# Performance work log

Hardware: AMD Instinct MI355X
Metric: run time of the kernel (lower is better)

Reference implementation:

```python
import jax, jax.numpy as jnp
import numpy as np

NH = 8          # num_heads (init kwarg)
NUM_GROUPS = 32
EPS = 1e-5


def setup_inputs() -> dict:
    key = jax.random.key(0)
    ks = jax.random.split(key, 4)
    B, C, H, W = 2, 512, 64, 64
    x = jax.random.normal(ks[0], (B, C, H, W), dtype=jnp.float32)
    qkv_w = jax.random.normal(ks[1], (3 * C, C), dtype=jnp.float32) * (1.0 / np.sqrt(C))
    proj_w = jax.random.normal(ks[2], (C, C), dtype=jnp.float32) * (1.0 / np.sqrt(C))
    proj_b = jax.random.normal(ks[3], (C,), dtype=jnp.float32) * 0.02
    gn_w = jnp.ones((C,), dtype=jnp.float32)
    gn_b = jnp.zeros((C,), dtype=jnp.float32)
    return {"x": x, "qkv_w": qkv_w, "proj_w": proj_w, "proj_b": proj_b,
            "gn_w": gn_w, "gn_b": gn_b}


def _group_norm(x, gamma, beta):
    B, C, H, W = x.shape
    xg = x.reshape(B, NUM_GROUPS, C // NUM_GROUPS, H, W)
    mean = xg.mean(axis=(2, 3, 4), keepdims=True)
    var = xg.var(axis=(2, 3, 4), keepdims=True)
    xg = (xg - mean) * jax.lax.rsqrt(var + EPS)
    x = xg.reshape(B, C, H, W)
    return x * gamma[None, :, None, None] + beta[None, :, None, None]


def reference(x, qkv_w, proj_w, proj_b, gn_w, gn_b):
    B, C, H, W = x.shape
    h = _group_norm(x, gn_w, gn_b)
    # 1x1 conv == channel matmul
    qkv = jnp.einsum('oc,bchw->bohw', qkv_w, h)  # [B, 3C, H, W]
    # faithful legacy reshape: per-head contiguous [q,k,v] blocks of 3*C//NH channels
    qkv = qkv.reshape(B * NH, 3 * C // NH, H * W)
    q, k, v = jnp.split(qkv, 3, axis=1)          # each [B*NH, C//NH, HW]
    scale = 1.0 / np.sqrt(np.sqrt(C // NH))
    attn = jnp.einsum('bci,bcj->bij', q * scale, k * scale)  # [B*NH, HW, HW]
    attn = jax.nn.softmax(attn, axis=-1)
    hout = jnp.einsum('bij,bcj->bci', attn, v)   # [B*NH, C//NH, HW]
    hout = hout.reshape(B, C, H, W)
    hout = jnp.einsum('oc,bchw->bohw', proj_w, hout) + proj_b[None, :, None, None]
    return x + hout
```

## Files before the change

kernel.cpp:

```cpp
#include <hip/hip_runtime.h>
#include <math.h>

typedef __attribute__((ext_vector_type(8))) short short8;
typedef __attribute__((ext_vector_type(4))) float floatx4;
typedef __attribute__((ext_vector_type(16))) float floatx16;

__device__ __forceinline__ unsigned short f2bf(float f) {
  union { float f; unsigned int u; } v; v.f = f;
  unsigned int r = v.u + 0x7fffu + ((v.u >> 16) & 1u);
  return (unsigned short)(r >> 16);
}

__device__ __forceinline__ float bf2f(unsigned short h) {
  union { unsigned int u; float f; } v; v.u = ((unsigned int)h) << 16;
  return v.f;
}

__device__ __forceinline__ unsigned int pack2(unsigned short a, unsigned short b) {
  return (unsigned int)a | ((unsigned int)b << 16);
}

__device__ __forceinline__ float fast_exp2(float x) {
#if __has_builtin(__builtin_amdgcn_exp2f)
  return __builtin_amdgcn_exp2f(x);
#else
  return exp2f(x);
#endif
}

__device__ __forceinline__ void async16(const unsigned short* gp, unsigned short* lp) {
  __builtin_amdgcn_global_load_lds(
      (__attribute__((address_space(1))) void*)(gp),
      (__attribute__((address_space(3))) void*)(lp), 16, 0, 0);
}

__global__ void setup_kernel(const float* __restrict__ x, float2* __restrict__ stats_p,
                             const float* __restrict__ qkv_w, unsigned short* __restrict__ wqkv,
                             const float* __restrict__ proj_w, unsigned short* __restrict__ wproj) {
  if (blockIdx.x < 512) {
    const int bid = blockIdx.x;
    const int bg  = bid >> 3;
    const int sub = bid & 7;
    const float4* p = (const float4*)(x + (size_t)bg * 65536 + (size_t)sub * 8192);
    float s = 0.f, ss = 0.f;
    #pragma unroll
    for (int i = 0; i < 8; i++) {
      float4 v = p[threadIdx.x + i*256];
      s  += v.x + v.y + v.z + v.w;
      ss += v.x*v.x + v.y*v.y + v.z*v.z + v.w*v.w;
    }
    #pragma unroll
    for (int off = 32; off >= 1; off >>= 1) {
      s  += __shfl_xor(s,  off, 64);
      ss += __shfl_xor(ss, off, 64);
    }
    __shared__ float red[2][4];
    int wv = threadIdx.x >> 6;
    if ((threadIdx.x & 63) == 0) { red[0][wv] = s; red[1][wv] = ss; }
    __syncthreads();
    if (threadIdx.x == 0) {
      s  = red[0][0] + red[0][1] + red[0][2] + red[0][3];
      ss = red[1][0] + red[1][1] + red[1][2] + red[1][3];
      stats_p[bid] = make_float2(s, ss);
    }
  } else {
    int i = (blockIdx.x - 512) * 256 + threadIdx.x;
    const float* s; unsigned short* d;
    if (i < 196608) { s = qkv_w; d = wqkv; }
    else { i -= 196608; s = proj_w; d = wproj; }
    float4 vv = ((const float4*)s)[i];
    uint2 o;
    o.x = pack2(f2bf(vv.x), f2bf(vv.y));
    o.y = pack2(f2bf(vv.z), f2bf(vv.w));
    ((uint2*)d)[i] = o;
  }
}

__global__ void gn_apply_t(const float* __restrict__ x, const float2* __restrict__ stats_p,
                           const float* __restrict__ gw, const float* __restrict__ gb,
                           unsigned short* __restrict__ h_t) {
  __shared__ __align__(16) unsigned short tile[64][72];
  const int b = blockIdx.z, c0 = blockIdx.y * 64, hw0 = blockIdx.x * 64;
  const int t = threadIdx.x;
  {
    const int cl = t >> 2;
    const int hs = (t & 3) * 16;
    const int c  = c0 + cl;
    const int g  = c >> 4;
    const float2* sp = stats_p + ((size_t)(b*32 + g) << 3);
    float s = 0.f, ss = 0.f;
    #pragma unroll
    for (int k = 0; k < 8; k++) { float2 v = sp[k]; s += v.x; ss += v.y; }
    const float mean = s * (1.f/65536.f);
    const float var  = ss * (1.f/65536.f) - mean*mean;
    const float rstd = rsqrtf(var + 1e-5f);
    const float w  = gw[c] * rstd;
    const float bb = gb[c] - mean * w;
    const float4* src = (const float4*)(x + ((size_t)(b*512 + c))*4096 + hw0 + hs);
    #pragma unroll
    for (int i = 0; i < 4; i++) {
      float4 vv = src[i];
      unsigned short* d = &tile[cl][hs + i*4];
      d[0] = f2bf(vv.x*w + bb); d[1] = f2bf(vv.y*w + bb);
      d[2] = f2bf(vv.z*w + bb); d[3] = f2bf(vv.w*w + bb);
    }
  }
  __syncthreads();
  {
    const int hwl = t >> 2;
    const int cs  = (t & 3) * 16;
    uint4 w0, w1;
    w0.x = pack2(tile[cs+ 0][hwl], tile[cs+ 1][hwl]);
    w0.y = pack2(tile[cs+ 2][hwl], tile[cs+ 3][hwl]);
    w0.z = pack2(tile[cs+ 4][hwl], tile[cs+ 5][hwl]);
    w0.w = pack2(tile[cs+ 6][hwl], tile[cs+ 7][hwl]);
    w1.x = pack2(tile[cs+ 8][hwl], tile[cs+ 9][hwl]);
    w1.y = pack2(tile[cs+10][hwl], tile[cs+11][hwl]);
    w1.z = pack2(tile[cs+12][hwl], tile[cs+13][hwl]);
    w1.w = pack2(tile[cs+14][hwl], tile[cs+15][hwl]);
    unsigned short* dst = h_t + ((size_t)(b*4096 + hw0 + hwl))*512 + c0 + cs;
    *(uint4*)dst       = w0;
    *(uint4*)(dst + 8) = w1;
  }
}

__global__ __launch_bounds__(256, 3)
void qkv_gemm(const unsigned short* __restrict__ A,
              const unsigned short* __restrict__ Bt,
              unsigned short* __restrict__ q_t,
              unsigned short* __restrict__ k_t,
              unsigned short* __restrict__ v_) {
  __shared__ __align__(16) unsigned short As[128*32];
  __shared__ __align__(16) unsigned short Bs[128*32];
  const int b   = blockIdx.z;
  const int n0  = blockIdx.x * 128;
  const int o0  = blockIdx.y * 128;
  const int tid = threadIdx.x;
  const int wave = tid >> 6, lane = tid & 63;
  const int wr = wave >> 1, wc = wave & 1;
  const int fm = lane & 15, fq = lane >> 4;
  const int srow = lane >> 2, scol = (lane & 3) * 8;

  const unsigned short* Ab = A + (size_t)o0 * 512;
  const unsigned short* Bb = Bt + ((size_t)b*4096 + n0) * 512;

  bool vsw[4];
  #pragma unroll
  for (int fr = 0; fr < 4; fr++) {
    const int ob = o0 + wr*64 + fr*16;
    vsw[fr] = ((ob % 192) >> 6) == 2;
  }

  floatx4 acc[4][4];
  #pragma unroll
  for (int i = 0; i < 4; i++)
    #pragma unroll
    for (int j = 0; j < 4; j++) acc[i][j] = (floatx4){0.f,0.f,0.f,0.f};

  for (int k0 = 0; k0 < 512; k0 += 32) {
    __syncthreads();
    #pragma unroll
    for (int cc = 0; cc < 2; cc++) {
      int ch = wave*2 + cc;
      async16(Ab + (size_t)(ch*16 + srow)*512 + k0 + scol, &As[ch*512]);
      async16(Bb + (size_t)(ch*16 + srow)*512 + k0 + scol, &Bs[ch*512]);
    }
    __syncthreads();
    short8 af[4], bf[4];
    #pragma unroll
    for (int f = 0; f < 4; f++) {
      af[f] = *(const short8*)&As[(wr*64 + f*16 + fm)*32 + fq*8];
      bf[f] = *(const short8*)&Bs[(wc*64 + f*16 + fm)*32 + fq*8];
    }
    #pragma unroll
    for (int fr = 0; fr < 4; fr++) {
      if (vsw[fr]) {
        #pragma unroll
        for (int fc = 0; fc < 4; fc++)
          acc[fr][fc] = __builtin_amdgcn_mfma_f32_16x16x32_bf16(bf[fc], af[fr], acc[fr][fc], 0, 0, 0);
      } else {
        #pragma unroll
        for (int fc = 0; fc < 4; fc++)
          acc[fr][fc] = __builtin_amdgcn_mfma_f32_16x16x32_bf16(af[fr], bf[fc], acc[fr][fc], 0, 0, 0);
      }
    }
  }

  #pragma unroll
  for (int fr = 0; fr < 4; fr++) {
    const int ob     = o0 + wr*64 + fr*16;
    const int head   = ob / 192;
    const int rem    = ob % 192;
    const int region = rem >> 6;
    const int bhh    = b*8 + head;
    #pragma unroll
    for (int fc = 0; fc < 4; fc++) {
      if (region == 0) {
        const int i = n0 + wc*64 + fc*16 + fm;
        const int dsub = (rem & 63) + fq*4;
        unsigned short t4[4];
        #pragma unroll
        for (int r = 0; r < 4; r++) t4[r] = f2bf(acc[fr][fc][r] * 0.18033688f);
        uint2 o; o.x = pack2(t4[0], t4[1]); o.y = pack2(t4[2], t4[3]);
        *(uint2*)&q_t[((size_t)bhh*4096 + i)*64 + dsub] = o;
      } else if (region == 1) {
        const int i = n0 + wc*64 + fc*16 + fm;
        const int dsub = (rem & 63) + fq*4;
        unsigned short t4[4];
        #pragma unroll
        for (int r = 0; r < 4; r++) t4[r] = f2bf(acc[fr][fc][r]);
        uint2 o; o.x = pack2(t4[0], t4[1]); o.y = pack2(t4[2], t4[3]);
        *(uint2*)&k_t[((size_t)bhh*4096 + i)*64 + dsub] = o;
      } else {
        const int dsub = (rem & 63) + fm;
        const int tok0 = n0 + wc*64 + fc*16 + fq*4;
        unsigned short t4[4];
        #pragma unroll
        for (int r = 0; r < 4; r++) t4[r] = f2bf(acc[fr][fc][r]);
        uint2 o; o.x = pack2(t4[0], t4[1]); o.y = pack2(t4[2], t4[3]);
        *(uint2*)&v_[((size_t)bhh*64 + dsub)*4096 + tok0] = o;
      }
    }
  }
}

__global__ __launch_bounds__(256, 2)
void proj_gemm(const unsigned short* __restrict__ A,
               const unsigned short* __restrict__ Bt,
               float* __restrict__ outp,
               const float* __restrict__ xres,
               const float* __restrict__ pbias) {
  __shared__ __align__(16) unsigned short As[64*32];
  __shared__ __align__(16) unsigned short Bs[128*32];
  const int b   = blockIdx.z;
  const int n0  = blockIdx.x * 128;
  const int o0  = blockIdx.y * 64;
  const int tid = threadIdx.x;
  const int wave = tid >> 6, lane = tid & 63;
  const int wr = wave >> 1, wc = wave & 1;
  const int fm = lane & 15, fq = lane >> 4;
  const int srow = lane >> 2, scol = (lane & 3) * 8;

  const unsigned short* Ab = A + (size_t)o0 * 512;
  const unsigned short* Bb = Bt + ((size_t)b*4096 + n0) * 512;

  floatx4 acc[2][4];
  #pragma unroll
  for (int i = 0; i < 2; i++)
    #pragma unroll
    for (int j = 0; j < 4; j++) acc[i][j] = (floatx4){0.f,0.f,0.f,0.f};

  for (int k0 = 0; k0 < 512; k0 += 32) {
    __syncthreads();
    async16(Ab + (size_t)(wave*16 + srow)*512 + k0 + scol, &As[wave*512]);
    #pragma unroll
    for (int cc = 0; cc < 2; cc++) {
      int ch = wave*2 + cc;
      async16(Bb + (size_t)(ch*16 + srow)*512 + k0 + scol, &Bs[ch*512]);
    }
    __syncthreads();
    short8 af[2], bf[4];
    #pragma unroll
    for (int f = 0; f < 2; f++)
      af[f] = *(const short8*)&As[(wr*32 + f*16 + fm)*32 + fq*8];
    #pragma unroll
    for (int f = 0; f < 4; f++)
      bf[f] = *(const short8*)&Bs[(wc*64 + f*16 + fm)*32 + fq*8];
    #pragma unroll
    for (int fr = 0; fr < 2; fr++)
      #pragma unroll
      for (int fc = 0; fc < 4; fc++)
        acc[fr][fc] = __builtin_amdgcn_mfma_f32_16x16x32_bf16(af[fr], bf[fc], acc[fr][fc], 0, 0, 0);
  }

  #pragma unroll
  for (int fr = 0; fr < 2; fr++)
    #pragma unroll
    for (int fc = 0; fc < 4; fc++) {
      const int i = n0 + wc*64 + fc*16 + fm;
      #pragma unroll
      for (int r = 0; r < 4; r++) {
        const int o = o0 + wr*32 + fr*16 + fq*4 + r;
        const size_t idx = ((size_t)b*512 + o)*4096 + i;
        outp[idx] = xres[idx] + pbias[o] + acc[fr][fc][r];
      }
    }
}


__device__ __forceinline__ void plswap(unsigned &a, unsigned &b) {
  asm("v_permlane32_swap_b32 %0, %1" : "+v"(a), "+v"(b));
}

__device__ __forceinline__ floatx16 qk4(const short8* kf, const short8* qf) {
  const floatx16 z16 = {0.f,0.f,0.f,0.f,0.f,0.f,0.f,0.f,
                        0.f,0.f,0.f,0.f,0.f,0.f,0.f,0.f};
  floatx16 st = __builtin_amdgcn_mfma_f32_32x32x16_bf16(kf[0], qf[0], z16, 0, 0, 0);
  #pragma unroll
  for (int kc = 1; kc < 4; kc++)
    st = __builtin_amdgcn_mfma_f32_32x32x16_bf16(kf[kc], qf[kc], st, 0, 0, 0);
  return st;
}

__device__ __forceinline__ void sm8(const floatx16 st, unsigned* pk, float2& lp) {
  #pragma unroll
  for (int rp = 0; rp < 8; rp++) {
    float p0 = fast_exp2(st[2*rp]);
    float p1 = fast_exp2(st[2*rp + 1]);
    lp.x += p0; lp.y += p1;
    unsigned r;
    asm("v_cvt_pk_bf16_f32 %0, %1, %2" : "=v"(r) : "v"(p0), "v"(p1));
    pk[rp] = r;
  }
}

__device__ __forceinline__ void pv16(const unsigned* pk,
                                     const short8 vA0, const short8 vA1,
                                     const short8 vB0, const short8 vB1,
                                     floatx16* o) {
  unsigned a0 = pk[0], a2 = pk[2]; plswap(a0, a2);
  unsigned a1 = pk[1], a3 = pk[3]; plswap(a1, a3);
  unsigned b0 = pk[4], b2 = pk[6]; plswap(b0, b2);
  unsigned b1 = pk[5], b3 = pk[7]; plswap(b1, b3);
  union { unsigned u[4]; short8 s; } lo, hi;
  lo.u[0] = a0; lo.u[1] = a1; lo.u[2] = a2; lo.u[3] = a3;
  hi.u[0] = b0; hi.u[1] = b1; hi.u[2] = b2; hi.u[3] = b3;
  o[0] = __builtin_amdgcn_mfma_f32_32x32x16_bf16(lo.s, vA0, o[0], 0, 0, 0);
  o[0] = __builtin_amdgcn_mfma_f32_32x32x16_bf16(hi.s, vB0, o[0], 0, 0, 0);
  o[1] = __builtin_amdgcn_mfma_f32_32x32x16_bf16(lo.s, vA1, o[1], 0, 0, 0);
  o[1] = __builtin_amdgcn_mfma_f32_32x32x16_bf16(hi.s, vB1, o[1], 0, 0, 0);
}

template <int NSPLIT>
__global__ __launch_bounds__(256, 2)
void attn_kernel(const unsigned short* __restrict__ q_t,
                 const unsigned short* __restrict__ k_t,
                 const unsigned short* __restrict__ v_,
                 unsigned short* __restrict__ hout_t,
                 unsigned short* __restrict__ o_part,
                 float* __restrict__ l_part) {
  __shared__ __align__(16) unsigned short Ks[2][64*72];
  __shared__ __align__(16) unsigned short Vs[2][64*72];

  const int bh  = blockIdx.x;
  const int q0  = blockIdx.y * 256;
  const int js  = (NSPLIT > 1) ? blockIdx.z : 0;
  const int nt  = 64 / NSPLIT;
  const int jbase = js * (4096 / NSPLIT);
  const int tid = threadIdx.x;
  const int wave = tid >> 6, lane = tid & 63;
  const int ln = lane & 31, h = lane >> 5;

  short8 qf[2][4];
  #pragma unroll
  for (int ih = 0; ih < 2; ih++) {
    const unsigned short* qrow = q_t + ((size_t)bh*4096 + q0 + wave*64 + ih*32 + ln)*64;
    #pragma unroll
    for (int kc = 0; kc < 4; kc++)
      qf[ih][kc] = *(const short8*)(qrow + kc*16 + h*8);
  }

  const floatx16 z16 = {0.f,0.f,0.f,0.f,0.f,0.f,0.f,0.f,
                        0.f,0.f,0.f,0.f,0.f,0.f,0.f,0.f};
  floatx16 o_acc[2][2];
  #pragma unroll
  for (int ih = 0; ih < 2; ih++) { o_acc[ih][0] = z16; o_acc[ih][1] = z16; }
  float2 lp0 = {0.f, 0.f}, lp1 = {0.f, 0.f};

  const int sr = tid >> 3;
  const int sc = (tid & 7) * 8;
  const unsigned short* kbase = k_t + (size_t)bh*262144;
  const unsigned short* vbase = v_  + (size_t)bh*262144;

  uint4 kr0 = *(const uint4*)&kbase[(size_t)(jbase + sr)*64 + sc];
  uint4 kr1 = *(const uint4*)&kbase[(size_t)(jbase + sr + 32)*64 + sc];
  uint4 vr0 = *(const uint4*)&vbase[(size_t)sr*4096 + jbase + sc];
  uint4 vr1 = *(const uint4*)&vbase[(size_t)(sr+32)*4096 + jbase + sc];

  for (int it = 0; it < nt; it++) {
    unsigned short* Kc = Ks[it & 1];
    unsigned short* Vc = Vs[it & 1];
    *(uint4*)&Kc[sr*72 + sc]      = kr0;
    *(uint4*)&Kc[(sr+32)*72 + sc] = kr1;
    *(uint4*)&Vc[sr*72 + sc]      = vr0;
    *(uint4*)&Vc[(sr+32)*72 + sc] = vr1;
    __syncthreads();

    {
      int itn = it + 1; if (itn == nt) itn = 0;
      const int jn = jbase + itn * 64;
      kr0 = *(const uint4*)&kbase[(size_t)(jn + sr)*64 + sc];
      kr1 = *(const uint4*)&kbase[(size_t)(jn + sr + 32)*64 + sc];
      vr0 = *(const uint4*)&vbase[(size_t)sr*4096 + jn + sc];
      vr1 = *(const uint4*)&vbase[(size_t)(sr+32)*4096 + jn + sc];
    }

    short8 kf0[4];
    #pragma unroll
    for (int kc = 0; kc < 4; kc++)
      kf0[kc] = *(const short8*)&Kc[(0*32 + ln)*72 + kc*16 + h*8];
    short8 vA0[2], vB0[2];
    #pragma unroll
    for (int dn = 0; dn < 2; dn++) {
      vA0[dn] = *(const short8*)&Vc[(dn*32 + ln)*72 + 0*32 + h*8];
      vB0[dn] = *(const short8*)&Vc[(dn*32 + ln)*72 + 0*32 + 16 + h*8];
    }

    floatx16 stA = qk4(kf0, qf[0]);

    floatx16 stB = qk4(kf0, qf[1]);
    unsigned pkA[8];
    sm8(stA, pkA, lp0);
    pv16(pkA, vA0[0], vA0[1], vB0[0], vB0[1], o_acc[0]);

    short8 kf1[4];
    #pragma unroll
    for (int kc = 0; kc < 4; kc++)
      kf1[kc] = *(const short8*)&Kc[(1*32 + ln)*72 + kc*16 + h*8];
    floatx16 stC = qk4(kf1, qf[0]);
    unsigned pkB[8];
    sm8(stB, pkB, lp1);
    pv16(pkB, vA0[0], vA0[1], vB0[0], vB0[1], o_acc[1]);

    short8 vA1[2], vB1[2];
    #pragma unroll
    for (int dn = 0; dn < 2; dn++) {
      vA1[dn] = *(const short8*)&Vc[(dn*32 + ln)*72 + 1*32 + h*8];
      vB1[dn] = *(const short8*)&Vc[(dn*32 + ln)*72 + 1*32 + 16 + h*8];
    }
    floatx16 stD = qk4(kf1, qf[1]);
    unsigned pkC[8];
    sm8(stC, pkC, lp0);
    pv16(pkC, vA1[0], vA1[1], vB1[0], vB1[1], o_acc[0]);

    unsigned pkD[8];
    sm8(stD, pkD, lp1);
    pv16(pkD, vA1[0], vA1[1], vB1[0], vB1[1], o_acc[1]);
  }

  float l0 = lp0.x + lp0.y;
  float l1 = lp1.x + lp1.y;
  l0 += __shfl_xor(l0, 32, 64);
  l1 += __shfl_xor(l1, 32, 64);

  if (NSPLIT > 1) {
    #pragma unroll
    for (int ih = 0; ih < 2; ih++) {
      unsigned short* op = o_part +
          (((size_t)(js*16 + bh)*4096 + q0 + wave*64 + ih*32) * 64);
      #pragma unroll
      for (int r = 0; r < 16; r++) {
        const int il = (r & 3) + 8*(r >> 2) + 4*h;
        op[(size_t)il*64 + ln]      = f2bf(o_acc[ih][0][r]);
        op[(size_t)il*64 + 32 + ln] = f2bf(o_acc[ih][1][r]);
      }
    }
    if (lane < 32) {
      l_part[(size_t)(js*16 + bh)*4096 + q0 + wave*64 + lane]      = l0;
      l_part[(size_t)(js*16 + bh)*4096 + q0 + wave*64 + 32 + lane] = l1;
    }
  } else {
    const float linv0 = 1.f / l0;
    const float linv1 = 1.f / l1;
    const int bb = bh >> 3;
    const int cb = (bh & 7) * 64;
    #pragma unroll
    for (int ih = 0; ih < 2; ih++) {
      #pragma unroll
      for (int r = 0; r < 16; r++) {
        const int il = (r & 3) + 8*(r >> 2) + 4*h;
        const float inv = __shfl(ih ? linv1 : linv0, il, 64);
        const int i = q0 + wave*64 + ih*32 + il;
        unsigned short* dst = &hout_t[((size_t)bb*4096 + i)*512 + cb + ln];
        dst[0]  = f2bf(o_acc[ih][0][r] * inv);
        dst[32] = f2bf(o_acc[ih][1][r] * inv);
      }
    }
  }
}

__global__ void attn_combine(const unsigned short* __restrict__ o_part,
                             const float* __restrict__ l_part,
                             unsigned short* __restrict__ hout_t) {
  const int bh = blockIdx.x;
  const int i0 = blockIdx.y * 64;
  const int t  = threadIdx.x;
  const int d4 = (t & 15) * 4;
  const int il = t >> 4;
  const int bb = bh >> 3;
  const int cb = (bh & 7) * 64;
  const size_t JS = (size_t)16 * 4096 * 64;
  #pragma unroll
  for (int p = 0; p < 4; p++) {
    const int i = i0 + p*16 + il;
    const size_t ob = ((size_t)bh*4096 + i)*64 + d4;
    uint2 a = *(const uint2*)&o_part[ob];
    uint2 b = *(const uint2*)&o_part[ob + JS];
    const size_t lb = (size_t)bh*4096 + i;
    const float inv = 1.f / (l_part[lb] + l_part[lb + 65536]);
    float o0 = (bf2f((unsigned short)(a.x & 0xffff)) + bf2f((unsigned short)(b.x & 0xffff))) * inv;
    float o1 = (bf2f((unsigned short)(a.x >> 16))    + bf2f((unsigned short)(b.x >> 16)))    * inv;
    float o2 = (bf2f((unsigned short)(a.y & 0xffff)) + bf2f((unsigned short)(b.y & 0xffff))) * inv;
    float o3 = (bf2f((unsigned short)(a.y >> 16))    + bf2f((unsigned short)(b.y >> 16)))    * inv;
    uint2 w;
    w.x = pack2(f2bf(o0), f2bf(o1));
    w.y = pack2(f2bf(o2), f2bf(o3));
    *(uint2*)&hout_t[((size_t)bb*4096 + i)*512 + cb + d4] = w;
  }
}

extern "C" void kernel_launch(void* const* d_in, const int* in_sizes, int n_in,
                              void* d_out, int out_size, void* d_ws, size_t ws_size,
                              hipStream_t stream) {
  (void)in_sizes; (void)n_in; (void)out_size;
  const float* x      = (const float*)d_in[0];
  const float* qkv_w  = (const float*)d_in[1];
  const float* proj_w = (const float*)d_in[2];
  const float* proj_b = (const float*)d_in[3];
  const float* gn_w   = (const float*)d_in[4];
  const float* gn_b   = (const float*)d_in[5];
  float* out = (float*)d_out;

  char* ws = (char*)d_ws;
  unsigned short* h_t   = (unsigned short*)(ws);
  unsigned short* q_t   = (unsigned short*)(ws + ((size_t)8  << 20));
  unsigned short* k_t   = (unsigned short*)(ws + ((size_t)16 << 20));
  unsigned short* v_    = (unsigned short*)(ws + ((size_t)24 << 20));
  unsigned short* wqkv  = (unsigned short*)(ws + ((size_t)32 << 20));
  unsigned short* wproj = (unsigned short*)(ws + ((size_t)34 << 20));
  float2* stats_p       = (float2*)(ws + ((size_t)35 << 20));
  unsigned short* o_part = (unsigned short*)(ws + ((size_t)36 << 20));
  float* l_part          = (float*)(ws + ((size_t)52 << 20));
  unsigned short* hout_t = h_t;

  const bool split = ws_size >= (((size_t)52 << 20) + ((size_t)1 << 19));

  setup_kernel<<<dim3(1536), dim3(256), 0, stream>>>(x, stats_p, qkv_w, wqkv, proj_w, wproj);
  gn_apply_t<<<dim3(64, 8, 2), dim3(256), 0, stream>>>(x, stats_p, gn_w, gn_b, h_t);
  qkv_gemm<<<dim3(32, 12, 2), dim3(256), 0, stream>>>(wqkv, h_t, q_t, k_t, v_);
  if (split) {
    attn_kernel<2><<<dim3(16, 16, 2), dim3(256), 0, stream>>>(q_t, k_t, v_, nullptr,
                                                              o_part, l_part);
    attn_combine<<<dim3(16, 64), dim3(256), 0, stream>>>(o_part, l_part, hout_t);
  } else {
    attn_kernel<1><<<dim3(16, 16), dim3(256), 0, stream>>>(q_t, k_t, v_, hout_t,
                                                           nullptr, nullptr);
  }
  proj_gemm<<<dim3(32, 8, 2), dim3(256), 0, stream>>>(wproj, hout_t, out, x, proj_b);
}
```

Measured before the change: 194.7 us.

## Double-buffer LDS tiles in QKV and projection GEMMs with prefetch

Both GEMM kernels now keep two LDS buffers for the A and B tiles. Each iteration issues the async loads for the next K-slice before computing on the current one. This drops one barrier per iteration and lets global-to-LDS traffic overlap the MFMA work. In exchange, shared memory use doubles, which can lower how many blocks fit on each CU.

```diff
diff --git a/kernel.cpp b/kernel.cpp
--- a/kernel.cpp
+++ b/kernel.cpp
@@ -130,8 +130,8 @@
               unsigned short* __restrict__ q_t,
               unsigned short* __restrict__ k_t,
               unsigned short* __restrict__ v_) {
-  __shared__ __align__(16) unsigned short As[128*32];
-  __shared__ __align__(16) unsigned short Bs[128*32];
+  __shared__ __align__(16) unsigned short As[2][128*32];
+  __shared__ __align__(16) unsigned short Bs[2][128*32];
   const int b   = blockIdx.z;
   const int n0  = blockIdx.x * 128;
   const int o0  = blockIdx.y * 128;
@@ -157,20 +157,32 @@
     #pragma unroll
     for (int j = 0; j < 4; j++) acc[i][j] = (floatx4){0.f,0.f,0.f,0.f};
 
-  for (int k0 = 0; k0 < 512; k0 += 32) {
+  #pragma unroll
+  for (int cc = 0; cc < 2; cc++) {
+    int ch = wave*2 + cc;
+    async16(Ab + (size_t)(ch*16 + srow)*512 + scol, &As[0][ch*512]);
+    async16(Bb + (size_t)(ch*16 + srow)*512 + scol, &Bs[0][ch*512]);
+  }
+
+  for (int it = 0; it < 16; it++) {
     __syncthreads();
-    #pragma unroll
-    for (int cc = 0; cc < 2; cc++) {
-      int ch = wave*2 + cc;
-      async16(Ab + (size_t)(ch*16 + srow)*512 + k0 + scol, &As[ch*512]);
-      async16(Bb + (size_t)(ch*16 + srow)*512 + k0 + scol, &Bs[ch*512]);
-    }
-    __syncthreads();
+    if (it < 15) {
+      const int k0 = (it + 1) * 32;
+      const int nb = (it + 1) & 1;
+      #pragma unroll
+      for (int cc = 0; cc < 2; cc++) {
+        int ch = wave*2 + cc;
+        async16(Ab + (size_t)(ch*16 + srow)*512 + k0 + scol, &As[nb][ch*512]);
+        async16(Bb + (size_t)(ch*16 + srow)*512 + k0 + scol, &Bs[nb][ch*512]);
+      }
+    }
+    const unsigned short* Ac = As[it & 1];
+    const unsigned short* Bc = Bs[it & 1];
     short8 af[4], bf[4];
     #pragma unroll
     for (int f = 0; f < 4; f++) {
-      af[f] = *(const short8*)&As[(wr*64 + f*16 + fm)*32 + fq*8];
-      bf[f] = *(const short8*)&Bs[(wc*64 + f*16 + fm)*32 + fq*8];
+      af[f] = *(const short8*)&Ac[(wr*64 + f*16 + fm)*32 + fq*8];
+      bf[f] = *(const short8*)&Bc[(wc*64 + f*16 + fm)*32 + fq*8];
     }
     #pragma unroll
     for (int fr = 0; fr < 4; fr++) {
@@ -230,8 +242,8 @@
                float* __restrict__ outp,
                const float* __restrict__ xres,
                const float* __restrict__ pbias) {
-  __shared__ __align__(16) unsigned short As[64*32];
-  __shared__ __align__(16) unsigned short Bs[128*32];
+  __shared__ __align__(16) unsigned short As[2][64*32];
+  __shared__ __align__(16) unsigned short Bs[2][128*32];
   const int b   = blockIdx.z;
   const int n0  = blockIdx.x * 128;
   const int o0  = blockIdx.y * 64;
@@ -250,22 +262,34 @@
     #pragma unroll
     for (int j = 0; j < 4; j++) acc[i][j] = (floatx4){0.f,0.f,0.f,0.f};
 
-  for (int k0 = 0; k0 < 512; k0 += 32) {
+  async16(Ab + (size_t)(wave*16 + srow)*512 + scol, &As[0][wave*512]);
+  #pragma unroll
+  for (int cc = 0; cc < 2; cc++) {
+    int ch = wave*2 + cc;
+    async16(Bb + (size_t)(ch*16 + srow)*512 + scol, &Bs[0][ch*512]);
+  }
+
+  for (int it = 0; it < 16; it++) {
     __syncthreads();
-    async16(Ab + (size_t)(wave*16 + srow)*512 + k0 + scol, &As[wave*512]);
-    #pragma unroll
-    for (int cc = 0; cc < 2; cc++) {
-      int ch = wave*2 + cc;
-      async16(Bb + (size_t)(ch*16 + srow)*512 + k0 + scol, &Bs[ch*512]);
-    }
-    __syncthreads();
+    if (it < 15) {
+      const int k0 = (it + 1) * 32;
+      const int nb = (it + 1) & 1;
+      async16(Ab + (size_t)(wave*16 + srow)*512 + k0 + scol, &As[nb][wave*512]);
+      #pragma unroll
+      for (int cc = 0; cc < 2; cc++) {
+        int ch = wave*2 + cc;
+        async16(Bb + (size_t)(ch*16 + srow)*512 + k0 + scol, &Bs[nb][ch*512]);
+      }
+    }
+    const unsigned short* Ac = As[it & 1];
+    const unsigned short* Bc = Bs[it & 1];
     short8 af[2], bf[4];
     #pragma unroll
     for (int f = 0; f < 2; f++)
-      af[f] = *(const short8*)&As[(wr*32 + f*16 + fm)*32 + fq*8];
+      af[f] = *(const short8*)&Ac[(wr*32 + f*16 + fm)*32 + fq*8];
     #pragma unroll
     for (int f = 0; f < 4; f++)
-      bf[f] = *(const short8*)&Bs[(wc*64 + f*16 + fm)*32 + fq*8];
+      bf[f] = *(const short8*)&Bc[(wc*64 + f*16 + fm)*32 + fq*8];
     #pragma unroll
     for (int fr = 0; fr < 2; fr++)
       #pragma unroll
```

Result: no change. 191.4 us (median of 2 runs) (-1.7%).
